# Kernel optimization log

Measured on AMD Instinct MI355X. Metric: run time of the kernel, lower is better.

Reference implementation:

```python
import jax, jax.numpy as jnp
import numpy as np
import math

T, B, D, H, FF = 2048, 2, 1024, 16, 4096
HD = D // H
STD = 0.02


def _gelu(x):
    # SongNet gelu: tanh approximation
    return 0.5 * x * (1.0 + jnp.tanh(math.sqrt(2.0 / math.pi) * (x + 0.044715 * x ** 3)))


def _layer_norm(x, g, b, eps=1e-5):
    mu = jnp.mean(x, axis=-1, keepdims=True)
    var = jnp.mean((x - mu) ** 2, axis=-1, keepdims=True)
    return (x - mu) * jax.lax.rsqrt(var + eps) * g + b


def setup_inputs() -> dict:
    key = jax.random.key(0)
    ks = jax.random.split(key, 6)
    return {
        "x": jax.random.normal(ks[0], (T, B, D), jnp.float32),
        "attn_mask": jnp.triu(jnp.ones((T, T), bool), k=1),  # True = masked (causal)
        "in_proj_w": jax.random.normal(ks[1], (3 * D, D), jnp.float32) * STD,
        "in_proj_b": jnp.zeros((3 * D,), jnp.float32),
        "out_w": jax.random.normal(ks[2], (D, D), jnp.float32) * STD,
        "out_b": jnp.zeros((D,), jnp.float32),
        "fc1_w": jax.random.normal(ks[3], (FF, D), jnp.float32) * STD,
        "fc1_b": jnp.zeros((FF,), jnp.float32),
        "fc2_w": jax.random.normal(ks[4], (D, FF), jnp.float32) * STD,
        "fc2_b": jnp.zeros((D,), jnp.float32),
        "ln1_g": jnp.ones((D,), jnp.float32),
        "ln1_b": jnp.zeros((D,), jnp.float32),
        "ln2_g": jnp.ones((D,), jnp.float32),
        "ln2_b": jnp.zeros((D,), jnp.float32),
    }


def reference(x, attn_mask, in_proj_w, in_proj_b, out_w, out_b,
              fc1_w, fc1_b, fc2_w, fc2_b, ln1_g, ln1_b, ln2_g, ln2_b):
    t, b, d = x.shape
    scaling = HD ** -0.5
    # fused in-proj (qkv_same path): [T,B,3D]
    qkv = x @ in_proj_w.T + in_proj_b
    q, k, v = jnp.split(qkv, 3, axis=-1)
    q = q * scaling

    def to_heads(z):  # [T,B,D] -> [B*H, T, HD]
        return z.reshape(t, b * H, HD).transpose(1, 0, 2)

    q, k, v = to_heads(q), to_heads(k), to_heads(v)
    # [B*H, T, T] attention scores (full matrix, as in original bmm)
    scores = jnp.einsum('nth,nsh->nts', q, k)
    scores = jnp.where(attn_mask[None, :, :], -jnp.inf, scores)
    w = jax.nn.softmax(scores, axis=-1)
    attn = jnp.einsum('nts,nsh->nth', w, v)          # [B*H, T, HD]
    attn = attn.transpose(1, 0, 2).reshape(t, b, d)  # [T,B,D]
    attn = attn @ out_w.T + out_b

    h = _layer_norm(x + attn, ln1_g, ln1_b)
    ff = _gelu(h @ fc1_w.T + fc1_b) @ fc2_w.T + fc2_b
    out = _layer_norm(h + ff, ln2_g, ln2_b)
    return out
```

## Files before the change

### kernel.cpp

```cpp
#include <hip/hip_runtime.h>
#include <hip/hip_bf16.h>
#include <math.h>


typedef __bf16 bf16x8_t __attribute__((ext_vector_type(8)));
typedef __bf16 bf16x4_t __attribute__((ext_vector_type(4)));
typedef float  f32x4_t  __attribute__((ext_vector_type(4)));

#define T_  2048
#define B_  2
#define D_  1024
#define H_  16
#define HD_ 64
#define FF_ 4096
#define M_  (T_ * B_)

#define LOG2E 1.4426950408889634f
#define SCL   (0.125f * LOG2E)

__device__ __forceinline__ float gelu_f(float v) {
    const float y = 0.79788456080286535588f * (v + 0.044715f * v * v * v);
    const float t = __builtin_amdgcn_exp2f(-2.8853900817779268f * y);
    return v * __builtin_amdgcn_rcpf(1.0f + t);
}

__device__ __forceinline__ void gld_lds16(const void* g, void* l) {
    __builtin_amdgcn_global_load_lds((const __attribute__((address_space(1))) void*)g,
                                     (__attribute__((address_space(3))) void*)l, 16, 0, 0);
}

template<int MODE, int OWNM>
__global__ __launch_bounds__(256, 4)
void gemm_bt(const __bf16* __restrict__ A, const __bf16* __restrict__ W,
             const float* __restrict__ bias, float* __restrict__ Cf0,
             float* __restrict__ Cf1, __bf16* __restrict__ Cb, int M, int N, int K)
{
    __shared__ __align__(16) __bf16 As[128 * 64];
    __shared__ __align__(16) __bf16 Bs[128 * 64];
    const int tid  = threadIdx.x;
    const int lane = tid & 63;
    const int wave = tid >> 6;
    const int quad = lane >> 4;
    const int l15  = lane & 15;

    const int gx = gridDim.x, gy = gridDim.y;
    int flat = ((int)blockIdx.z * gy + (int)blockIdx.y) * gx + (int)blockIdx.x;
    int bx, by, z;
    if (OWNM) {
        const int P = gy >> 3;
        const int x = flat & 7; int s = flat >> 3;
        by = x * P + (s % P); s /= P;
        bx = s % gx; z = s / gx;
    } else {
        const int P = gx >> 3;
        const int x = flat & 7; int s = flat >> 3;
        bx = x * P + (s % P); s /= P;
        by = s % gy; z = s / gy;
    }
    const int m0 = by * 128;
    const int n0 = bx * 128;
    const int wm = (wave >> 1) * 64;
    const int wn = (wave & 1) * 64;
    const int Kloc = K / (int)gridDim.z;
    const int kbeg = z * Kloc;

    const int srow8 = lane >> 3;
    const int scol  = ((lane & 7) ^ srow8) * 8;
    const __bf16* gA = A + (size_t)(m0 + wave * 32 + srow8) * K + scol;
    const __bf16* gB = W + (size_t)(n0 + wave * 32 + srow8) * K + scol;
    const size_t row8K = (size_t)8 * K;
    __bf16* ldsA = As + wave * 2048;
    __bf16* ldsB = Bs + wave * 2048;

    const int fsw = l15 & 7;

    f32x4_t acc[4][4] = {};

    for (int kb = kbeg; kb < kbeg + Kloc; kb += 64) {
        #pragma unroll
        for (int j = 0; j < 4; ++j) {
            gld_lds16(gA + kb + j * row8K, ldsA + j * 512);
            gld_lds16(gB + kb + j * row8K, ldsB + j * 512);
        }
        __syncthreads();
        #pragma unroll
        for (int half = 0; half < 2; ++half) {
            const int co = ((quad + half * 4) ^ fsw) * 8;
            bf16x8_t af[4], bfr[4];
            #pragma unroll
            for (int i = 0; i < 4; ++i) af[i]  = *(const bf16x8_t*)&As[(wm + i * 16 + l15) * 64 + co];
            #pragma unroll
            for (int i = 0; i < 4; ++i) bfr[i] = *(const bf16x8_t*)&Bs[(wn + i * 16 + l15) * 64 + co];
            #pragma unroll
            for (int mi = 0; mi < 4; ++mi)
                #pragma unroll
                for (int ni = 0; ni < 4; ++ni)
                    acc[mi][ni] = __builtin_amdgcn_mfma_f32_16x16x32_bf16(af[mi], bfr[ni], acc[mi][ni], 0, 0, 0);
        }
        __syncthreads();
    }

    float* __restrict__ Cf = (z == 0) ? Cf0 : Cf1;
    #pragma unroll
    for (int mi = 0; mi < 4; ++mi) {
        const int row = m0 + wm + mi * 16 + quad * 4;
        #pragma unroll
        for (int ni = 0; ni < 4; ++ni) {
            const int col = n0 + wn + ni * 16 + l15;
            const float bv = (z == 0) ? bias[col] : 0.f;
            #pragma unroll
            for (int r = 0; r < 4; ++r) {
                float v = acc[mi][ni][r] + bv;
                if (MODE == 2) v = gelu_f(v);
                if (MODE == 0) Cf[(size_t)(row + r) * N + col] = v;
                else           Cb[(size_t)(row + r) * N + col] = (__bf16)v;
            }
        }
    }
}

__global__ __launch_bounds__(256)
void vtrans_kernel(const __bf16* __restrict__ qkv, __bf16* __restrict__ vt)
{
    __shared__ __bf16 S[64][72];
    const int tt = blockIdx.x, bh = blockIdx.y;
    const int b = bh >> 4, h = bh & 15;
    const int tid = threadIdx.x;
    const int tl = tid >> 2, ch = (tid & 3) * 16;
    const __bf16* src = qkv + ((size_t)(tt * 64 + tl) * B_ + b) * (3 * D_) + 2 * D_ + h * HD_ + ch;
    *(bf16x8_t*)&S[tl][ch]     = *(const bf16x8_t*)src;
    *(bf16x8_t*)&S[tl][ch + 8] = *(const bf16x8_t*)(src + 8);
    __syncthreads();
    #pragma unroll
    for (int p = 0; p < 2; ++p) {
        const int hd = p * 32 + (tid >> 3);
        const int tc = (tid & 7) * 8;
        bf16x8_t v;
        #pragma unroll
        for (int j = 0; j < 8; ++j) v[j] = S[tc + j][hd];
        *(bf16x8_t*)(vt + ((size_t)bh * 64 + hd) * T_ + tt * 64 + tc) = v;
    }
}

struct QState {
    bf16x8_t aq0, aq1;
    f32x4_t  o[4];
    f32x4_t  lacc;
};

__device__ __forceinline__ void attn_tile_step(
    QState& st, const __bf16* __restrict__ Ks, const __bf16* __restrict__ Vs,
    __bf16* __restrict__ Psw, bool diag, int wave, int quad, int l15, int ksw)
{
    const bf16x8_t ONES = {(__bf16)1.f, (__bf16)1.f, (__bf16)1.f, (__bf16)1.f,
                           (__bf16)1.f, (__bf16)1.f, (__bf16)1.f, (__bf16)1.f};
    f32x4_t sc[4] = {};
    #pragma unroll
    for (int ni = 0; ni < 4; ++ni) {
        const int rb = (ni * 16 + l15) * 64;
        bf16x8_t kf0 = *(const bf16x8_t*)&Ks[rb + ((quad ^ ksw) & 7) * 8];
        bf16x8_t kf1 = *(const bf16x8_t*)&Ks[rb + (((quad + 4) ^ ksw) & 7) * 8];
        sc[ni] = __builtin_amdgcn_mfma_f32_16x16x32_bf16(st.aq0, kf0, sc[ni], 0, 0, 0);
        sc[ni] = __builtin_amdgcn_mfma_f32_16x16x32_bf16(st.aq1, kf1, sc[ni], 0, 0, 0);
    }
    #pragma unroll
    for (int ni = 0; ni < 4; ++ni) {
        #pragma unroll
        for (int r = 0; r < 4; ++r) {
            float pv = __builtin_amdgcn_exp2f(sc[ni][r] * SCL);
            if (diag) {
                const int tr_ = wave * 16 + quad * 4 + r;
                pv = ((ni * 16 + l15) <= tr_) ? pv : 0.f;
            }
            const int row = quad * 4 + r;
            const int ch = ((ni * 2 + (l15 >> 3)) + (row >> 1)) & 7;
            Psw[row * 64 + ch * 8 + (l15 & 7)] = (__bf16)pv;
        }
    }
    bf16x8_t ap0 = *(const bf16x8_t*)&Psw[l15 * 64 + ((quad + (l15 >> 1)) & 7) * 8];
    bf16x8_t ap1 = *(const bf16x8_t*)&Psw[l15 * 64 + ((quad + 4 + (l15 >> 1)) & 7) * 8];

    st.lacc = __builtin_amdgcn_mfma_f32_16x16x32_bf16(ap0, ONES, st.lacc, 0, 0, 0);
    st.lacc = __builtin_amdgcn_mfma_f32_16x16x32_bf16(ap1, ONES, st.lacc, 0, 0, 0);

    #pragma unroll
    for (int ni = 0; ni < 4; ++ni) {
        const int rbv = (ni * 16 + l15) * 64;
        bf16x8_t bv0 = *(const bf16x8_t*)&Vs[rbv + ((quad ^ ksw) & 7) * 8];
        bf16x8_t bv1 = *(const bf16x8_t*)&Vs[rbv + (((quad + 4) ^ ksw) & 7) * 8];
        st.o[ni] = __builtin_amdgcn_mfma_f32_16x16x32_bf16(ap0, bv0, st.o[ni], 0, 0, 0);
        st.o[ni] = __builtin_amdgcn_mfma_f32_16x16x32_bf16(ap1, bv1, st.o[ni], 0, 0, 0);
    }
}

__global__ __launch_bounds__(256)
void attn_kernel(const __bf16* __restrict__ qkv, const __bf16* __restrict__ vt,
                 __bf16* __restrict__ attnout)
{
    const int bh = blockIdx.y;
    const int b  = bh >> 4;
    const int h  = bh & 15;
    const int tid  = threadIdx.x;
    const int lane = tid & 63;
    const int wave = tid >> 6;
    const int quad = lane >> 4;
    const int l15  = lane & 15;

    __shared__ __align__(16) __bf16 Ks[64 * 64];
    __shared__ __align__(16) __bf16 Vs[64 * 64];
    __shared__ __align__(16) __bf16 Ps[4][16 * 64];

    const int kr = lane >> 3;
    const int kc = (lane & 7) ^ kr;
    const size_t krow = (size_t)B_ * 3 * D_;
    const __bf16* gK0 = qkv + ((size_t)(wave * 16 + kr) * B_ + b) * (3 * D_) + D_ + h * HD_ + kc * 8;
    const __bf16* gV0 = vt + ((size_t)bh * 64 + wave * 16 + kr) * T_ + kc * 8;
    __bf16* ldsK0 = &Ks[wave * 16 * 64];
    __bf16* ldsK1 = &Ks[wave * 16 * 64 + 8 * 64];
    __bf16* ldsV0 = &Vs[wave * 16 * 64];
    __bf16* ldsV1 = &Vs[wave * 16 * 64 + 8 * 64];
    const int ksw = l15 & 7;
    __bf16* Psw = &Ps[wave][0];

    const int qtA = 31 - (int)blockIdx.x;
    const int qtB = (int)blockIdx.x;

    QState stA = {}, stB = {};
    {
        const int tqA = qtA * 64 + wave * 16 + l15;
        const __bf16* qbA = qkv + ((size_t)tqA * B_ + b) * (3 * D_) + h * HD_;
        stA.aq0 = *(const bf16x8_t*)(qbA + quad * 8);
        stA.aq1 = *(const bf16x8_t*)(qbA + 32 + quad * 8);
        const int tqB = qtB * 64 + wave * 16 + l15;
        const __bf16* qbB = qkv + ((size_t)tqB * B_ + b) * (3 * D_) + h * HD_;
        stB.aq0 = *(const bf16x8_t*)(qbB + quad * 8);
        stB.aq1 = *(const bf16x8_t*)(qbB + 32 + quad * 8);
    }

    for (int kt = 0; kt <= qtA; ++kt) {
        const int s0 = kt * 64;
        __syncthreads();
        gld_lds16(gK0 + (size_t)s0 * krow,       ldsK0);
        gld_lds16(gK0 + (size_t)(s0 + 8) * krow, ldsK1);
        gld_lds16(gV0 + s0,                      ldsV0);
        gld_lds16(gV0 + (size_t)8 * T_ + s0,     ldsV1);
        __syncthreads();

        attn_tile_step(stA, Ks, Vs, Psw, kt == qtA, wave, quad, l15, ksw);
        if (kt <= qtB)
            attn_tile_step(stB, Ks, Vs, Psw, kt == qtB, wave, quad, l15, ksw);
    }

    #pragma unroll
    for (int t = 0; t < 2; ++t) {
        const QState& st = t ? stB : stA;
        const int q0 = (t ? qtB : qtA) * 64;
        float linv[4];
        #pragma unroll
        for (int r = 0; r < 4; ++r) linv[r] = __builtin_amdgcn_rcpf(st.lacc[r]);
        #pragma unroll
        for (int ni = 0; ni < 4; ++ni) {
            #pragma unroll
            for (int r = 0; r < 4; ++r) {
                const int tr = q0 + wave * 16 + quad * 4 + r;
                attnout[((size_t)tr * B_ + b) * D_ + h * HD_ + ni * 16 + l15] =
                    (__bf16)(st.o[ni][r] * linv[r]);
            }
        }
    }
}

__global__ __launch_bounds__(256)
void ln3_kernel(const float* __restrict__ A, const float* __restrict__ R0,
                const float* __restrict__ R1,
                const float* __restrict__ g, const float* __restrict__ bb,
                float* __restrict__ outf, __bf16* __restrict__ outb)
{
    const int row = blockIdx.x;
    const int tid = threadIdx.x;
    const float4 va = ((const float4*)(A  + (size_t)row * D_))[tid];
    const float4 v0 = ((const float4*)(R0 + (size_t)row * D_))[tid];
    const float4 v1 = ((const float4*)(R1 + (size_t)row * D_))[tid];
    const float z0 = va.x + v0.x + v1.x, z1 = va.y + v0.y + v1.y;
    const float z2 = va.z + v0.z + v1.z, z3 = va.w + v0.w + v1.w;
    float s  = z0 + z1 + z2 + z3;
    float ss = z0 * z0 + z1 * z1 + z2 * z2 + z3 * z3;
    #pragma unroll
    for (int off = 1; off < 64; off <<= 1) {
        s  += __shfl_xor(s, off, 64);
        ss += __shfl_xor(ss, off, 64);
    }
    __shared__ float rs[4], rss[4];
    const int wv = tid >> 6, lane = tid & 63;
    if (lane == 0) { rs[wv] = s; rss[wv] = ss; }
    __syncthreads();
    s  = rs[0] + rs[1] + rs[2] + rs[3];
    ss = rss[0] + rss[1] + rss[2] + rss[3];
    const float mu   = s * (1.f / D_);
    const float var  = ss * (1.f / D_) - mu * mu;
    const float rstd = rsqrtf(var + 1e-5f);
    const float4 vg = ((const float4*)g)[tid];
    const float4 vb = ((const float4*)bb)[tid];
    const float o0 = (z0 - mu) * rstd * vg.x + vb.x;
    const float o1 = (z1 - mu) * rstd * vg.y + vb.y;
    const float o2 = (z2 - mu) * rstd * vg.z + vb.z;
    const float o3 = (z3 - mu) * rstd * vg.w + vb.w;
    ((float4*)(outf + (size_t)row * D_))[tid] = make_float4(o0, o1, o2, o3);
    if (outb) {
        bf16x4_t ob;
        ob[0] = (__bf16)o0; ob[1] = (__bf16)o1; ob[2] = (__bf16)o2; ob[3] = (__bf16)o3;
        ((bf16x4_t*)(outb + (size_t)row * D_))[tid] = ob;
    }
}

__global__ __launch_bounds__(256)
void cvt3_kernel(const float* __restrict__ s0, __bf16* __restrict__ d0, int n0,
                 const float* __restrict__ s1, __bf16* __restrict__ d1, int n1,
                 const float* __restrict__ s2, __bf16* __restrict__ d2, int n2)
{
    int i = blockIdx.x * 256 + threadIdx.x;
    const float* s; __bf16* d;
    if (i < n0) { s = s0; d = d0; }
    else if ((i -= n0) < n1) { s = s1; d = d1; }
    else if ((i -= n1) < n2) { s = s2; d = d2; }
    else return;
    const float4 v = ((const float4*)s)[i];
    bf16x4_t ob;
    ob[0] = (__bf16)v.x; ob[1] = (__bf16)v.y; ob[2] = (__bf16)v.z; ob[3] = (__bf16)v.w;
    ((bf16x4_t*)d)[i] = ob;
}

extern "C" void kernel_launch(void* const* d_in, const int* in_sizes, int n_in,
                              void* d_out, int out_size, void* d_ws, size_t ws_size,
                              hipStream_t stream)
{
    (void)in_sizes; (void)n_in; (void)out_size; (void)ws_size;
    const float* x         = (const float*)d_in[0];
    const float* in_proj_w = (const float*)d_in[2];
    const float* in_proj_b = (const float*)d_in[3];
    const float* out_w     = (const float*)d_in[4];
    const float* out_b     = (const float*)d_in[5];
    const float* fc1_w     = (const float*)d_in[6];
    const float* fc1_b     = (const float*)d_in[7];
    const float* fc2_w     = (const float*)d_in[8];
    const float* fc2_b     = (const float*)d_in[9];
    const float* ln1_g     = (const float*)d_in[10];
    const float* ln1_b     = (const float*)d_in[11];
    const float* ln2_g     = (const float*)d_in[12];
    const float* ln2_b     = (const float*)d_in[13];

    char* p = (char*)d_ws;
    __bf16* regA = (__bf16*)p; p += (size_t)M_ * D_ * 2;
    __bf16* hb   = (__bf16*)p; p += (size_t)M_ * D_ * 2;
    float*  yf2  = (float*)regA;
    __bf16* wreg = (__bf16*)p; p += (size_t)FF_ * D_ * 2;
    __bf16* qkvb = (__bf16*)p;
    __bf16* g1b  = qkvb;       p += (size_t)M_ * FF_ * 2;
    float*  yf   = (float*)p;  p += (size_t)M_ * D_ * 4;
    float*  hf   = (float*)p;  p += (size_t)M_ * D_ * 4;
    __bf16* vt   = (__bf16*)yf;
    __bf16* outwb = wreg + (size_t)3 * D_ * D_;

    const dim3 blk(256);

    {
        const int nx = M_ * D_ / 4, ni = 3 * D_ * D_ / 4, no = D_ * D_ / 4;
        cvt3_kernel<<<dim3((nx + ni + no) / 256), blk, 0, stream>>>(
            x, regA, nx, in_proj_w, wreg, ni, out_w, outwb, no);
    }

    gemm_bt<1, 1><<<dim3(3 * D_ / 128, M_ / 128, 1), blk, 0, stream>>>(
        regA, wreg, in_proj_b, nullptr, nullptr, qkvb, M_, 3 * D_, D_);

    vtrans_kernel<<<dim3(T_ / 64, B_ * H_), blk, 0, stream>>>(qkvb, vt);
    attn_kernel<<<dim3(T_ / 128, B_ * H_), blk, 0, stream>>>(qkvb, vt, regA);

    gemm_bt<0, 1><<<dim3(D_ / 128, M_ / 128, 2), blk, 0, stream>>>(
        regA, outwb, out_b, yf, hf, nullptr, M_, D_, D_);

    ln3_kernel<<<dim3(M_), blk, 0, stream>>>(x, yf, hf, ln1_g, ln1_b, hf, hb);

    cvt3_kernel<<<dim3((FF_ * D_ / 4) / 256), blk, 0, stream>>>(
        fc1_w, wreg, FF_ * D_ / 4, nullptr, nullptr, 0, nullptr, nullptr, 0);
    gemm_bt<2, 0><<<dim3(FF_ / 128, M_ / 128, 1), blk, 0, stream>>>(
        hb, wreg, fc1_b, nullptr, nullptr, g1b, M_, FF_, D_);

    cvt3_kernel<<<dim3((D_ * FF_ / 4) / 256), blk, 0, stream>>>(
        fc2_w, wreg, D_ * FF_ / 4, nullptr, nullptr, 0, nullptr, nullptr, 0);
    gemm_bt<0, 1><<<dim3(D_ / 128, M_ / 128, 2), blk, 0, stream>>>(
        g1b, wreg, fc2_b, yf, yf2, nullptr, M_, D_, FF_);

    ln3_kernel<<<dim3(M_), blk, 0, stream>>>(hf, yf, yf2, ln2_g, ln2_b, (float*)d_out, nullptr);
}
```

Measured before the change: 351.2 us.

## Fuse V transpose into QKV GEMM, transpose attention scores, merge weight casts

Removes the separate V-transpose kernel: the QKV GEMM epilogue now writes V directly in transposed layout. The attention step computes transposed scores, so the row sums come from shuffles instead of an MFMA against a ones vector, and the P staging layout in LDS changes to match. The two FFN weight conversions are merged into one launch. LN1 no longer writes the fp32 copy of h, and LN2 reads the bf16 copy as its residual, which saves bandwidth but lowers the residual's precision. Buffers are reassigned, including d_out used as scratch for the FC2 split-K output.

Result: faster. 329.1 us (-6.3%).

```diff
diff --git a/kernel.cpp b/kernel.cpp
--- a/kernel.cpp
+++ b/kernel.cpp
@@ -5,6 +5,7 @@
 
 typedef __bf16 bf16x8_t __attribute__((ext_vector_type(8)));
 typedef __bf16 bf16x4_t __attribute__((ext_vector_type(4)));
+typedef __bf16 bf16x2_t __attribute__((ext_vector_type(2)));
 typedef float  f32x4_t  __attribute__((ext_vector_type(4)));
 
 #define T_  2048
@@ -29,11 +30,12 @@
                                      (__attribute__((address_space(3))) void*)l, 16, 0, 0);
 }
 
-template<int MODE, int OWNM>
+template<int MODE, int OWNM, int VT>
 __global__ __launch_bounds__(256, 4)
 void gemm_bt(const __bf16* __restrict__ A, const __bf16* __restrict__ W,
              const float* __restrict__ bias, float* __restrict__ Cf0,
-             float* __restrict__ Cf1, __bf16* __restrict__ Cb, int M, int N, int K)
+             float* __restrict__ Cf1, __bf16* __restrict__ Cb,
+             __bf16* __restrict__ vt, int M, int N, int K)
 {
     __shared__ __align__(16) __bf16 As[128 * 64];
     __shared__ __align__(16) __bf16 Bs[128 * 64];
@@ -108,80 +110,78 @@
         for (int ni = 0; ni < 4; ++ni) {
             const int col = n0 + wn + ni * 16 + l15;
             const float bv = (z == 0) ? bias[col] : 0.f;
+            float v[4];
             #pragma unroll
             for (int r = 0; r < 4; ++r) {
-                float v = acc[mi][ni][r] + bv;
-                if (MODE == 2) v = gelu_f(v);
-                if (MODE == 0) Cf[(size_t)(row + r) * N + col] = v;
-                else           Cb[(size_t)(row + r) * N + col] = (__bf16)v;
+                v[r] = acc[mi][ni][r] + bv;
+                if (MODE == 2) v[r] = gelu_f(v[r]);
+            }
+            if (MODE == 0) {
+                #pragma unroll
+                for (int r = 0; r < 4; ++r) Cf[(size_t)(row + r) * N + col] = v[r];
+            } else {
+                #pragma unroll
+                for (int r = 0; r < 4; ++r) Cb[(size_t)(row + r) * N + col] = (__bf16)v[r];
+            }
+            if (VT && n0 >= 2 * D_) {
+                const int colv = col - 2 * D_;
+                const int h2 = colv >> 6, hd = colv & 63;
+                const int t0 = row >> 1;
+                bf16x2_t p0 = {(__bf16)v[0], (__bf16)v[2]};
+                bf16x2_t p1 = {(__bf16)v[1], (__bf16)v[3]};
+                *(bf16x2_t*)(vt + ((size_t)(h2 * 64 + hd)) * T_ + t0) = p0;
+                *(bf16x2_t*)(vt + ((size_t)((H_ + h2) * 64 + hd)) * T_ + t0) = p1;
             }
         }
-    }
-}
-
-__global__ __launch_bounds__(256)
-void vtrans_kernel(const __bf16* __restrict__ qkv, __bf16* __restrict__ vt)
-{
-    __shared__ __bf16 S[64][72];
-    const int tt = blockIdx.x, bh = blockIdx.y;
-    const int b = bh >> 4, h = bh & 15;
-    const int tid = threadIdx.x;
-    const int tl = tid >> 2, ch = (tid & 3) * 16;
-    const __bf16* src = qkv + ((size_t)(tt * 64 + tl) * B_ + b) * (3 * D_) + 2 * D_ + h * HD_ + ch;
-    *(bf16x8_t*)&S[tl][ch]     = *(const bf16x8_t*)src;
-    *(bf16x8_t*)&S[tl][ch + 8] = *(const bf16x8_t*)(src + 8);
-    __syncthreads();
-    #pragma unroll
-    for (int p = 0; p < 2; ++p) {
-        const int hd = p * 32 + (tid >> 3);
-        const int tc = (tid & 7) * 8;
-        bf16x8_t v;
-        #pragma unroll
-        for (int j = 0; j < 8; ++j) v[j] = S[tc + j][hd];
-        *(bf16x8_t*)(vt + ((size_t)bh * 64 + hd) * T_ + tt * 64 + tc) = v;
     }
 }
 
 struct QState {
     bf16x8_t aq0, aq1;
     f32x4_t  o[4];
-    f32x4_t  lacc;
+    float    lsum;
 };
 
 __device__ __forceinline__ void attn_tile_step(
     QState& st, const __bf16* __restrict__ Ks, const __bf16* __restrict__ Vs,
     __bf16* __restrict__ Psw, bool diag, int wave, int quad, int l15, int ksw)
 {
-    const bf16x8_t ONES = {(__bf16)1.f, (__bf16)1.f, (__bf16)1.f, (__bf16)1.f,
-                           (__bf16)1.f, (__bf16)1.f, (__bf16)1.f, (__bf16)1.f};
-    f32x4_t sc[4] = {};
+    f32x4_t scT[4] = {};
     #pragma unroll
     for (int ni = 0; ni < 4; ++ni) {
         const int rb = (ni * 16 + l15) * 64;
         bf16x8_t kf0 = *(const bf16x8_t*)&Ks[rb + ((quad ^ ksw) & 7) * 8];
         bf16x8_t kf1 = *(const bf16x8_t*)&Ks[rb + (((quad + 4) ^ ksw) & 7) * 8];
-        sc[ni] = __builtin_amdgcn_mfma_f32_16x16x32_bf16(st.aq0, kf0, sc[ni], 0, 0, 0);
-        sc[ni] = __builtin_amdgcn_mfma_f32_16x16x32_bf16(st.aq1, kf1, sc[ni], 0, 0, 0);
-    }
+        scT[ni] = __builtin_amdgcn_mfma_f32_16x16x32_bf16(kf0, st.aq0, scT[ni], 0, 0, 0);
+        scT[ni] = __builtin_amdgcn_mfma_f32_16x16x32_bf16(kf1, st.aq1, scT[ni], 0, 0, 0);
+    }
+    float rsum = 0.f;
     #pragma unroll
     for (int ni = 0; ni < 4; ++ni) {
+        bf16x4_t pk;
         #pragma unroll
         for (int r = 0; r < 4; ++r) {
-            float pv = __builtin_amdgcn_exp2f(sc[ni][r] * SCL);
+            float pv = __builtin_amdgcn_exp2f(scT[ni][r] * SCL);
             if (diag) {
-                const int tr_ = wave * 16 + quad * 4 + r;
-                pv = ((ni * 16 + l15) <= tr_) ? pv : 0.f;
+                const int sl = ni * 16 + quad * 4 + r;
+                pv = (sl <= wave * 16 + l15) ? pv : 0.f;
             }
-            const int row = quad * 4 + r;
-            const int ch = ((ni * 2 + (l15 >> 3)) + (row >> 1)) & 7;
-            Psw[row * 64 + ch * 8 + (l15 & 7)] = (__bf16)pv;
+            rsum += pv;
+            pk[r] = (__bf16)pv;
         }
-    }
-    bf16x8_t ap0 = *(const bf16x8_t*)&Psw[l15 * 64 + ((quad + (l15 >> 1)) & 7) * 8];
-    bf16x8_t ap1 = *(const bf16x8_t*)&Psw[l15 * 64 + ((quad + 4 + (l15 >> 1)) & 7) * 8];
-
-    st.lacc = __builtin_amdgcn_mfma_f32_16x16x32_bf16(ap0, ONES, st.lacc, 0, 0, 0);
-    st.lacc = __builtin_amdgcn_mfma_f32_16x16x32_bf16(ap1, ONES, st.lacc, 0, 0, 0);
+        *(bf16x4_t*)&Psw[l15 * 64 + ((ni * 4 + quad + l15) & 15) * 4] = pk;
+    }
+    rsum += __shfl_xor(rsum, 16, 64);
+    rsum += __shfl_xor(rsum, 32, 64);
+    st.lsum += rsum;
+
+    const int rowb = l15 * 64;
+    bf16x4_t a0 = *(const bf16x4_t*)&Psw[rowb + ((quad * 2     + l15) & 15) * 4];
+    bf16x4_t a1 = *(const bf16x4_t*)&Psw[rowb + ((quad * 2 + 1 + l15) & 15) * 4];
+    bf16x4_t a2 = *(const bf16x4_t*)&Psw[rowb + ((quad * 2 + 8 + l15) & 15) * 4];
+    bf16x4_t a3 = *(const bf16x4_t*)&Psw[rowb + ((quad * 2 + 9 + l15) & 15) * 4];
+    bf16x8_t ap0 = __builtin_shufflevector(a0, a1, 0, 1, 2, 3, 4, 5, 6, 7);
+    bf16x8_t ap1 = __builtin_shufflevector(a2, a3, 0, 1, 2, 3, 4, 5, 6, 7);
 
     #pragma unroll
     for (int ni = 0; ni < 4; ++ni) {
@@ -257,7 +257,8 @@
         const int q0 = (t ? qtB : qtA) * 64;
         float linv[4];
         #pragma unroll
-        for (int r = 0; r < 4; ++r) linv[r] = __builtin_amdgcn_rcpf(st.lacc[r]);
+        for (int r = 0; r < 4; ++r)
+            linv[r] = __builtin_amdgcn_rcpf(__shfl(st.lsum, quad * 4 + r, 64));
         #pragma unroll
         for (int ni = 0; ni < 4; ++ni) {
             #pragma unroll
@@ -270,19 +271,27 @@
     }
 }
 
+template<int AF32, int WF, int WB>
 __global__ __launch_bounds__(256)
-void ln3_kernel(const float* __restrict__ A, const float* __restrict__ R0,
+void ln3_kernel(const void* __restrict__ Ap, const float* __restrict__ R0,
                 const float* __restrict__ R1,
                 const float* __restrict__ g, const float* __restrict__ bb,
                 float* __restrict__ outf, __bf16* __restrict__ outb)
 {
     const int row = blockIdx.x;
     const int tid = threadIdx.x;
-    const float4 va = ((const float4*)(A  + (size_t)row * D_))[tid];
+    float a0, a1, a2, a3;
+    if (AF32) {
+        const float4 va = ((const float4*)((const float*)Ap + (size_t)row * D_))[tid];
+        a0 = va.x; a1 = va.y; a2 = va.z; a3 = va.w;
+    } else {
+        const bf16x4_t va = ((const bf16x4_t*)((const __bf16*)Ap + (size_t)row * D_))[tid];
+        a0 = (float)va[0]; a1 = (float)va[1]; a2 = (float)va[2]; a3 = (float)va[3];
+    }
     const float4 v0 = ((const float4*)(R0 + (size_t)row * D_))[tid];
     const float4 v1 = ((const float4*)(R1 + (size_t)row * D_))[tid];
-    const float z0 = va.x + v0.x + v1.x, z1 = va.y + v0.y + v1.y;
-    const float z2 = va.z + v0.z + v1.z, z3 = va.w + v0.w + v1.w;
+    const float z0 = a0 + v0.x + v1.x, z1 = a1 + v0.y + v1.y;
+    const float z2 = a2 + v0.z + v1.z, z3 = a3 + v0.w + v1.w;
     float s  = z0 + z1 + z2 + z3;
     float ss = z0 * z0 + z1 * z1 + z2 * z2 + z3 * z3;
     #pragma unroll
@@ -305,8 +314,8 @@
     const float o1 = (z1 - mu) * rstd * vg.y + vb.y;
     const float o2 = (z2 - mu) * rstd * vg.z + vb.z;
     const float o3 = (z3 - mu) * rstd * vg.w + vb.w;
-    ((float4*)(outf + (size_t)row * D_))[tid] = make_float4(o0, o1, o2, o3);
-    if (outb) {
+    if (WF) ((float4*)(outf + (size_t)row * D_))[tid] = make_float4(o0, o1, o2, o3);
+    if (WB) {
         bf16x4_t ob;
         ob[0] = (__bf16)o0; ob[1] = (__bf16)o1; ob[2] = (__bf16)o2; ob[3] = (__bf16)o3;
         ((bf16x4_t*)(outb + (size_t)row * D_))[tid] = ob;
@@ -352,14 +361,15 @@
     char* p = (char*)d_ws;
     __bf16* regA = (__bf16*)p; p += (size_t)M_ * D_ * 2;
     __bf16* hb   = (__bf16*)p; p += (size_t)M_ * D_ * 2;
-    float*  yf2  = (float*)regA;
     __bf16* wreg = (__bf16*)p; p += (size_t)FF_ * D_ * 2;
     __bf16* qkvb = (__bf16*)p;
     __bf16* g1b  = qkvb;       p += (size_t)M_ * FF_ * 2;
     float*  yf   = (float*)p;  p += (size_t)M_ * D_ * 4;
     float*  hf   = (float*)p;  p += (size_t)M_ * D_ * 4;
-    __bf16* vt   = (__bf16*)yf;
+    __bf16* vt    = (__bf16*)yf;
     __bf16* outwb = wreg + (size_t)3 * D_ * D_;
+    __bf16* fc2wb = (__bf16*)hf;
+    float*  ff1   = (float*)d_out;
 
     const dim3 blk(256);
 
@@ -369,26 +379,24 @@
             x, regA, nx, in_proj_w, wreg, ni, out_w, outwb, no);
     }
 
-    gemm_bt<1, 1><<<dim3(3 * D_ / 128, M_ / 128, 1), blk, 0, stream>>>(
-        regA, wreg, in_proj_b, nullptr, nullptr, qkvb, M_, 3 * D_, D_);
-
-    vtrans_kernel<<<dim3(T_ / 64, B_ * H_), blk, 0, stream>>>(qkvb, vt);
+    gemm_bt<1, 1, 1><<<dim3(3 * D_ / 128, M_ / 128, 1), blk, 0, stream>>>(
+        regA, wreg, in_proj_b, nullptr, nullptr, qkvb, vt, M_, 3 * D_, D_);
+
     attn_kernel<<<dim3(T_ / 128, B_ * H_), blk, 0, stream>>>(qkvb, vt, regA);
 
-    gemm_bt<0, 1><<<dim3(D_ / 128, M_ / 128, 2), blk, 0, stream>>>(
-        regA, outwb, out_b, yf, hf, nullptr, M_, D_, D_);
-
-    ln3_kernel<<<dim3(M_), blk, 0, stream>>>(x, yf, hf, ln1_g, ln1_b, hf, hb);
-
-    cvt3_kernel<<<dim3((FF_ * D_ / 4) / 256), blk, 0, stream>>>(
-        fc1_w, wreg, FF_ * D_ / 4, nullptr, nullptr, 0, nullptr, nullptr, 0);
-    gemm_bt<2, 0><<<dim3(FF_ / 128, M_ / 128, 1), blk, 0, stream>>>(
-        hb, wreg, fc1_b, nullptr, nullptr, g1b, M_, FF_, D_);
-
-    cvt3_kernel<<<dim3((D_ * FF_ / 4) / 256), blk, 0, stream>>>(
-        fc2_w, wreg, D_ * FF_ / 4, nullptr, nullptr, 0, nullptr, nullptr, 0);
-    gemm_bt<0, 1><<<dim3(D_ / 128, M_ / 128, 2), blk, 0, stream>>>(
-        g1b, wreg, fc2_b, yf, yf2, nullptr, M_, D_, FF_);
-
-    ln3_kernel<<<dim3(M_), blk, 0, stream>>>(hf, yf, yf2, ln2_g, ln2_b, (float*)d_out, nullptr);
-}
+    gemm_bt<0, 1, 0><<<dim3(D_ / 128, M_ / 128, 2), blk, 0, stream>>>(
+        regA, outwb, out_b, yf, hf, nullptr, nullptr, M_, D_, D_);
+
+    ln3_kernel<1, 0, 1><<<dim3(M_), blk, 0, stream>>>(x, yf, hf, ln1_g, ln1_b, nullptr, hb);
+
+    cvt3_kernel<<<dim3((2 * FF_ * D_ / 4) / 256), blk, 0, stream>>>(
+        fc1_w, wreg, FF_ * D_ / 4, fc2_w, fc2wb, D_ * FF_ / 4, nullptr, nullptr, 0);
+
+    gemm_bt<2, 0, 0><<<dim3(FF_ / 128, M_ / 128, 1), blk, 0, stream>>>(
+        hb, wreg, fc1_b, nullptr, nullptr, g1b, nullptr, M_, FF_, D_);
+
+    gemm_bt<0, 1, 0><<<dim3(D_ / 128, M_ / 128, 2), blk, 0, stream>>>(
+        g1b, fc2wb, fc2_b, yf, ff1, nullptr, nullptr, M_, D_, FF_);
+
+    ln3_kernel<0, 1, 0><<<dim3(M_), blk, 0, stream>>>(hb, yf, ff1, ln2_g, ln2_b, (float*)d_out, nullptr);
+}
```
